# Optimization experiments

Hardware: AMD Instinct MI355X
Metric: run time of the kernel (lower is better)

## Reference

```python
import jax, jax.numpy as jnp
import numpy as np

N_NODES = 30000
N_EDGES = 240000
N_GRAPHS = 300
IN_CH = 5


def _bn(x, p):
    # inference batchnorm; p = stack([gamma, beta, running_mean, running_var]), shape (4, C)
    g, b, m, v = p
    return g * (x - m) * jax.lax.rsqrt(v + 1e-5) + b


def _gatv2(x, src, dst, wl, bl, wr, br, att, bias, heads, outc, concat):
    # PyG GATv2Conv: e_ij = att . leaky_relu(lin_l(x_j) + lin_r(x_i)), softmax over edges into i,
    # out_i = sum_j alpha_ij * lin_l(x_j)
    n = x.shape[0]
    xl = (x @ wl + bl).reshape(n, heads, outc)  # source-side transform
    xr = (x @ wr + br).reshape(n, heads, outc)  # target-side transform
    e = jax.nn.leaky_relu(xl[src] + xr[dst], 0.2)          # [E, H, C]
    logit = jnp.einsum('ehc,hc->eh', e, att)               # [E, H]
    lmax = jax.ops.segment_max(logit, dst, num_segments=n)
    lmax = jnp.where(jnp.isfinite(lmax), lmax, 0.0)        # empty segments -> 0
    ex = jnp.exp(logit - lmax[dst])
    den = jax.ops.segment_sum(ex, dst, num_segments=n)
    alpha = ex / (den[dst] + 1e-16)                        # PyG softmax eps
    out = jax.ops.segment_sum(xl[src] * alpha[..., None], dst, num_segments=n)
    out = out.reshape(n, heads * outc) if concat else out.mean(axis=1)
    return out + bias


def _forward(x, edge_index, batch, w_in, b_in, bn_in,
             g1_wl, g1_bl, g1_wr, g1_br, g1_att, g1_bias, bn1,
             g2_wl, g2_bl, g2_wr, g2_br, g2_att, g2_bias, bn2,
             g3_wl, g3_bl, g3_wr, g3_br, g3_att, g3_bias, bn3,
             c_w1, c_b1, c_bn, c_w2, c_b2, c_w3, c_b3):
    n = x.shape[0]
    loops = jnp.arange(n)
    src = jnp.concatenate([edge_index[0], loops])  # add_self_loops=True
    dst = jnp.concatenate([edge_index[1], loops])
    h = jax.nn.relu(_bn(x @ w_in + b_in, bn_in))
    h = jax.nn.elu(_bn(_gatv2(h, src, dst, g1_wl, g1_bl, g1_wr, g1_br, g1_att, g1_bias, 4, 64, True), bn1))
    h = jax.nn.elu(_bn(_gatv2(h, src, dst, g2_wl, g2_bl, g2_wr, g2_br, g2_att, g2_bias, 4, 64, True), bn2))
    h = jax.nn.elu(_bn(_gatv2(h, src, dst, g3_wl, g3_bl, g3_wr, g3_br, g3_att, g3_bias, 1, 128, False), bn3))
    cnt = jax.ops.segment_sum(jnp.ones((n,), h.dtype), batch, num_segments=N_GRAPHS)
    mean = jax.ops.segment_sum(h, batch, num_segments=N_GRAPHS) / jnp.maximum(cnt, 1.0)[:, None]
    mx = jax.ops.segment_max(h, batch, num_segments=N_GRAPHS)
    mx = jnp.where(jnp.isfinite(mx), mx, 0.0)
    g = jnp.concatenate([mean, mx], axis=1)                # (B, 256)
    z = jax.nn.relu(_bn(g @ c_w1 + c_b1, c_bn))
    z = jax.nn.relu(z @ c_w2 + c_b2)
    return jax.nn.log_softmax(z @ c_w3 + c_b3, axis=-1)    # (B, 2)


def setup_inputs() -> dict:
    base = jax.random.key(0)
    k = lambda i: jax.random.fold_in(base, i)
    def lin(i, fi, fo):
        return jax.random.normal(k(i), (fi, fo), jnp.float32) / np.sqrt(np.float32(fi))
    def vec(i, c):
        return jax.random.normal(k(i), (c,), jnp.float32) * 0.05
    def bn(i, c):
        g = jax.random.uniform(k(i), (c,), jnp.float32) + 0.5
        b = jax.random.normal(jax.random.fold_in(k(i), 1), (c,), jnp.float32) * 0.1
        return jnp.stack([g, b, jnp.zeros((c,), jnp.float32), jnp.ones((c,), jnp.float32)])
    def att(i, h, c):
        return jax.random.normal(k(i), (h, c), jnp.float32) / np.sqrt(np.float32(c))
    return dict(
        x=jax.random.normal(k(0), (N_NODES, IN_CH), jnp.float32),
        edge_index=jax.random.randint(k(1), (2, N_EDGES), 0, N_NODES),
        batch=jnp.sort(jax.random.randint(k(2), (N_NODES,), 0, N_GRAPHS)),
        w_in=lin(3, IN_CH, 64), b_in=vec(4, 64), bn_in=bn(5, 64),
        g1_wl=lin(6, 64, 256), g1_bl=vec(7, 256), g1_wr=lin(8, 64, 256), g1_br=vec(9, 256),
        g1_att=att(10, 4, 64), g1_bias=vec(11, 256), bn1=bn(12, 256),
        g2_wl=lin(13, 256, 256), g2_bl=vec(14, 256), g2_wr=lin(15, 256, 256), g2_br=vec(16, 256),
        g2_att=att(17, 4, 64), g2_bias=vec(18, 256), bn2=bn(19, 256),
        g3_wl=lin(20, 256, 128), g3_bl=vec(21, 128), g3_wr=lin(22, 256, 128), g3_br=vec(23, 128),
        g3_att=att(24, 1, 128), g3_bias=vec(25, 128), bn3=bn(26, 128),
        c_w1=lin(27, 256, 128), c_b1=vec(28, 128), c_bn=bn(29, 128),
        c_w2=lin(30, 128, 64), c_b2=vec(31, 64),
        c_w3=lin(32, 64, 2), c_b3=vec(33, 2),
    )


def reference(x, edge_index, batch, w_in, b_in, bn_in,
              g1_wl, g1_bl, g1_wr, g1_br, g1_att, g1_bias, bn1,
              g2_wl, g2_bl, g2_wr, g2_br, g2_att, g2_bias, bn2,
              g3_wl, g3_bl, g3_wr, g3_br, g3_att, g3_bias, bn3,
              c_w1, c_b1, c_bn, c_w2, c_b2, c_w3, c_b3):
    return _forward(x, edge_index, batch, w_in, b_in, bn_in,
                    g1_wl, g1_bl, g1_wr, g1_br, g1_att, g1_bias, bn1,
                    g2_wl, g2_bl, g2_wr, g2_br, g2_att, g2_bias, bn2,
                    g3_wl, g3_bl, g3_wr, g3_br, g3_att, g3_bias, bn3,
                    c_w1, c_b1, c_bn, c_w2, c_b2, c_w3, c_b3)
```

## Files before the change

### kernel.cpp

```cpp
#include <hip/hip_runtime.h>
#include <math.h>

#define N_NODES  30000
#define N_EDGES  240000
#define E_TOT    270000
#define N_GRAPHS 300
#define NCH      118

typedef _Float16 half8 __attribute__((ext_vector_type(8)));
typedef _Float16 half4 __attribute__((ext_vector_type(4)));
typedef float float4v __attribute__((ext_vector_type(4)));

static inline int cdiv(int a, int b) { return (a + b - 1) / b; }

static __device__ __forceinline__ void gload_lds16(const void* g, void* l) {
    __builtin_amdgcn_global_load_lds(
        (const __attribute__((address_space(1))) void*)g,
        (__attribute__((address_space(3))) void*)l, 16, 0, 0);
}

template<int CTRL>
static __device__ __forceinline__ float dpp_add(float v) {
    int t = __builtin_amdgcn_update_dpp(0, __float_as_int(v), CTRL, 0xF, 0xF, false);
    return v + __int_as_float(t);
}
static __device__ __forceinline__ float red16(float v) {
    v = dpp_add<0x128>(v);
    v = dpp_add<0x124>(v);
    v = dpp_add<0x122>(v);
    v = dpp_add<0x121>(v);
    return v;
}

__device__ inline void wp_dev(const float* __restrict__ W, _Float16* __restrict__ Wt,
                              int K, int CO, int gtid, int T) {
    int tot = K * CO;
    for (int i = gtid; i < tot; i += T) {
        int k = i / CO, c = i - k * CO;
        Wt[(size_t)c * K + k] = (_Float16)W[i];
    }
}

__global__ void hist_wprep_input(const int* __restrict__ ei, int* __restrict__ deg,
                                 const float* __restrict__ x, const float* __restrict__ w_in,
                                 const float* __restrict__ b_in, const float* __restrict__ bn_in,
                                 _Float16* __restrict__ a16,
                                 const float* __restrict__ w1l, const float* __restrict__ w1r,
                                 const float* __restrict__ w2l, const float* __restrict__ w2r,
                                 const float* __restrict__ w3l, const float* __restrict__ w3r,
                                 _Float16* __restrict__ t1l, _Float16* __restrict__ t1r,
                                 _Float16* __restrict__ t2l, _Float16* __restrict__ t2r,
                                 _Float16* __restrict__ t3l, _Float16* __restrict__ t3r) {
    int gtid = blockIdx.x * blockDim.x + threadIdx.x;
    int T = gridDim.x * blockDim.x;
    for (int e = gtid; e < E_TOT; e += T) {
        int d = (e < N_EDGES) ? ei[N_EDGES + e] : e - N_EDGES;
        atomicAdd(&deg[d], 1);
    }
    wp_dev(w1l, t1l, 64, 256, gtid, T);
    wp_dev(w1r, t1r, 64, 256, gtid, T);
    wp_dev(w2l, t2l, 256, 256, gtid, T);
    wp_dev(w2r, t2r, 256, 256, gtid, T);
    wp_dev(w3l, t3l, 256, 128, gtid, T);
    wp_dev(w3r, t3r, 256, 128, gtid, T);

    int lane = threadIdx.x & 63;
    int wv = blockIdx.x * (blockDim.x >> 6) + (threadIdx.x >> 6);
    int NW = gridDim.x * (blockDim.x >> 6);
    float g = bn_in[lane], be = bn_in[64 + lane];
    float m = bn_in[128 + lane], va = bn_in[192 + lane];
    float rs = rsqrtf(va + 1e-5f);
    float wcol[5];
#pragma unroll
    for (int ci = 0; ci < 5; ++ci) wcol[ci] = w_in[ci * 64 + lane];
    float bb = b_in[lane];
    for (int n = wv; n < N_NODES; n += NW) {
        float xv = (lane < 5) ? x[n * 5 + lane] : 0.f;
        float acc = bb;
#pragma unroll
        for (int ci = 0; ci < 5; ++ci)
            acc = fmaf(__shfl(xv, ci, 64), wcol[ci], acc);
        acc = g * (acc - m) * rs + be;
        a16[(size_t)n * 64 + lane] = (_Float16)fmaxf(acc, 0.f);
    }
}

__global__ __launch_bounds__(256)
void scan_all(const int* __restrict__ deg, const int* __restrict__ batch,
              int* __restrict__ row_start, int* __restrict__ gstart) {
    __shared__ int red[256];
    __shared__ int s[256];
    const int b = blockIdx.x, t = threadIdx.x;
    int pre = 0;
    for (int i = t; i < b * 256; i += 256) pre += deg[i];
    red[t] = pre;
    __syncthreads();
    for (int off = 128; off; off >>= 1) {
        if (t < off) red[t] += red[t + off];
        __syncthreads();
    }
    int base = red[0];
    int gid = b * 256 + t;
    int v = (gid < N_NODES) ? deg[gid] : 0;
    s[t] = v;
    __syncthreads();
    for (int off = 1; off < 256; off <<= 1) {
        int u = (t >= off) ? s[t - off] : 0;
        __syncthreads();
        s[t] += u;
        __syncthreads();
    }
    if (gid < N_NODES) row_start[gid] = base + s[t] - v;
    if (b == 0 && t == 0) row_start[N_NODES] = E_TOT;
    if (b == 0) {
        for (int g = t; g <= N_GRAPHS; g += 256) {
            int lo = 0, hi = N_NODES;
            while (lo < hi) {
                int mid = (lo + hi) >> 1;
                if (batch[mid] < g) lo = mid + 1;
                else                hi = mid;
            }
            gstart[g] = lo;
        }
    }
}

template<int K, int COUT, int SCAT>
__global__ __launch_bounds__(256, 4)
void gemm_mfma(const _Float16* __restrict__ A,
               const _Float16* __restrict__ Wtl, const float* __restrict__ bl,
               const _Float16* __restrict__ Wtr, const float* __restrict__ br,
               _Float16* __restrict__ outl, _Float16* __restrict__ outr,
               const int* __restrict__ ei, const int* __restrict__ row_start,
               int* __restrict__ cnt, int* __restrict__ esrc, int N) {
    constexpr int BM = 128, BN = 128, BK = 64;
    constexpr int CSL = COUT / BN > 0 ? COUT / BN : 1;
    constexpr int NS  = 2 * CSL;
    const int NT  = (N + BM - 1) / BM;
    const int nwg = NT * NS;
    const int id  = blockIdx.x;
    if (SCAT && id >= nwg) {
        int gtid = (id - nwg) * blockDim.x + threadIdx.x;
        int T = (gridDim.x - nwg) * blockDim.x;
        for (int e = gtid; e < E_TOT; e += T) {
            int s, d;
            if (e < N_EDGES) { s = ei[e]; d = ei[N_EDGES + e]; }
            else             { s = e - N_EDGES; d = s; }
            int slot = row_start[d] + atomicAdd(&cnt[d], 1);
            esrc[slot] = s;
        }
        return;
    }
    const int q = nwg >> 3, r = nwg & 7, xcd = id & 7, kk_ = id >> 3;
    const int rm = (xcd < r ? xcd * (q + 1) : r * (q + 1) + (xcd - r) * q) + kk_;
    const int tile = rm / NS, slice = rm % NS;

    __shared__ __attribute__((aligned(16))) _Float16 As[BM * BK];
    __shared__ __attribute__((aligned(16))) _Float16 Bs[BN * BK];
    const int tid  = threadIdx.x;
    const int wave = tid >> 6;
    const int lane = tid & 63;
    const int l15  = lane & 15;
    const int lq   = lane >> 4;
    const int n0   = tile * BM;
    const int sel  = slice / CSL;
    const int col0 = (slice % CSL) * BN;
    const _Float16* Wt = sel ? Wtr : Wtl;
    const float* bias  = sel ? br : bl;
    _Float16* out      = sel ? outr : outl;

    const int r0 = tid >> 3;
    const int us = (tid & 7) ^ (r0 & 7);

    float4v acc[2][8];
#pragma unroll
    for (int mi = 0; mi < 2; ++mi)
#pragma unroll
        for (int nt = 0; nt < 8; ++nt)
#pragma unroll
            for (int r2 = 0; r2 < 4; ++r2) acc[mi][nt][r2] = 0.f;

    for (int kt = 0; kt < K; kt += BK) {
#pragma unroll
        for (int p = 0; p < 4; ++p) {
            int row = p * 32 + r0;
            int gn  = n0 + row;
            if (gn >= N) gn = 0;
            gload_lds16(A + (size_t)gn * K + kt + us * 8, As + (p * 256 + tid) * 8);
        }
#pragma unroll
        for (int p = 0; p < 4; ++p) {
            int row = p * 32 + r0;
            gload_lds16(Wt + (size_t)(col0 + row) * K + kt + us * 8, Bs + (p * 256 + tid) * 8);
        }
        __syncthreads();
#pragma unroll
        for (int kk = 0; kk < BK; kk += 32) {
            const int sw = (lq + (kk >> 3)) ^ (l15 & 7);
            half8 af0 = *(const half8*)(As + (wave * 32 + l15) * BK + sw * 8);
            half8 af1 = *(const half8*)(As + (wave * 32 + 16 + l15) * BK + sw * 8);
#pragma unroll
            for (int nt = 0; nt < 8; ++nt) {
                half8 bf = *(const half8*)(Bs + (nt * 16 + l15) * BK + sw * 8);
                acc[0][nt] = __builtin_amdgcn_mfma_f32_16x16x32_f16(bf, af0, acc[0][nt], 0, 0, 0);
                acc[1][nt] = __builtin_amdgcn_mfma_f32_16x16x32_f16(bf, af1, acc[1][nt], 0, 0, 0);
            }
        }
        __syncthreads();
    }
#pragma unroll
    for (int mi = 0; mi < 2; ++mi) {
        int row = n0 + wave * 32 + mi * 16 + l15;
        if (row < N) {
#pragma unroll
            for (int nt = 0; nt < 8; ++nt) {
                int col = col0 + nt * 16 + lq * 4;
                float4v bv = *(const float4v*)(bias + col);
                half4 hv;
#pragma unroll
                for (int r2 = 0; r2 < 4; ++r2)
                    hv[r2] = (_Float16)(acc[mi][nt][r2] + bv[r2]);
                *(half4*)(out + (size_t)row * COUT + col) = hv;
            }
        }
    }
}

template<typename TOUT>
__global__ __launch_bounds__(256)
void gat_gather4(const _Float16* __restrict__ xl, const _Float16* __restrict__ xr,
                 const int* __restrict__ row_start, const int* __restrict__ esrc,
                 const float* __restrict__ att, const float* __restrict__ gbias,
                 const float* __restrict__ bnp, TOUT* __restrict__ out) {
    constexpr int HC = 256, PER = 4;
    int node = (blockIdx.x * blockDim.x + threadIdx.x) >> 6;
    int lane = threadIdx.x & 63;
    if (node >= N_NODES) return;
    const int base = lane * PER;

    float rr[PER], av[PER], acc[PER];
    {
        half4 rv = *(const half4*)(xr + (size_t)node * HC + base);
#pragma unroll
        for (int k = 0; k < PER; ++k) rr[k] = (float)rv[k];
        *(float4v*)av = *(const float4v*)(att + base);
    }
#pragma unroll
    for (int k = 0; k < PER; ++k) acc[k] = 0.f;

    float l = 0.f;
    const int j0 = row_start[node], j1 = row_start[node + 1];
    for (int jc = j0; jc < j1; jc += 64) {
        int nedge = min(64, j1 - jc);
        int ev = (jc + lane < j1) ? esrc[jc + lane] : 0;
        for (int jj = 0; jj < nedge; jj += 4) {
            int s[4];
            bool val[4];
#pragma unroll
            for (int u = 0; u < 4; ++u) {
                int idx = jj + u;
                val[u] = idx < nedge;
                s[u] = __shfl(ev, val[u] ? idx : jj, 64);
            }
            float xs[4][PER];
#pragma unroll
            for (int u = 0; u < 4; ++u) {
                half4 xv = *(const half4*)(xl + (size_t)s[u] * HC + base);
#pragma unroll
                for (int k = 0; k < PER; ++k) xs[u][k] = (float)xv[k];
            }
            float pz[4];
#pragma unroll
            for (int u = 0; u < 4; ++u) {
                float pp = 0.f;
#pragma unroll
                for (int k = 0; k < PER; ++k) {
                    float v = xs[u][k] + rr[k];
                    v = (v > 0.f) ? v : 0.2f * v;
                    pp = fmaf(v, av[k], pp);
                }
                pz[u] = red16(pp);
            }
            float w[4];
#pragma unroll
            for (int u = 0; u < 4; ++u) w[u] = val[u] ? __expf(pz[u]) : 0.f;
            l += (w[0] + w[1]) + (w[2] + w[3]);
#pragma unroll
            for (int k = 0; k < PER; ++k)
                acc[k] += fmaf(w[0], xs[0][k],
                          fmaf(w[1], xs[1][k],
                          fmaf(w[2], xs[2][k], w[3] * xs[3][k])));
        }
    }
    float inv = 1.f / (l + 1e-16f);
    float o[PER];
#pragma unroll
    for (int k = 0; k < PER; ++k) {
        float v = fmaf(acc[k], inv, gbias[base + k]);
        float g  = bnp[base + k], be = bnp[HC + base + k];
        float mm = bnp[2 * HC + base + k], va = bnp[3 * HC + base + k];
        v = g * (v - mm) * rsqrtf(va + 1e-5f) + be;
        o[k] = (v > 0.f) ? v : (__expf(v) - 1.f);
    }
    half4 ov;
#pragma unroll
    for (int k = 0; k < PER; ++k) ov[k] = (_Float16)o[k];
    *(half4*)((_Float16*)out + (size_t)node * HC + base) = ov;
}

__global__ __launch_bounds__(256)
void gat_gather1(const _Float16* __restrict__ xl, const _Float16* __restrict__ xr,
                 const int* __restrict__ row_start, const int* __restrict__ esrc,
                 const float* __restrict__ att, const float* __restrict__ gbias,
                 const float* __restrict__ bnp, float* __restrict__ out) {
    constexpr int HC = 128, PER = 4;
    int node = (blockIdx.x * blockDim.x + threadIdx.x) >> 6;
    int lane = threadIdx.x & 63;
    if (node >= N_NODES) return;
    const int half = lane >> 5;
    const int base = (lane & 31) * PER;

    float rr[PER], av[PER], acc[PER];
    {
        half4 rv = *(const half4*)(xr + (size_t)node * HC + base);
#pragma unroll
        for (int k = 0; k < PER; ++k) rr[k] = (float)rv[k];
        *(float4v*)av = *(const float4v*)(att + base);
    }
#pragma unroll
    for (int k = 0; k < PER; ++k) acc[k] = 0.f;

    float l = 0.f;
    const int j0 = row_start[node], j1 = row_start[node + 1];
    for (int jc = j0; jc < j1; jc += 64) {
        int nedge = min(64, j1 - jc);
        int ev = (jc + lane < j1) ? esrc[jc + lane] : 0;
        for (int jj = 0; jj < nedge; jj += 8) {
            int s[4];
            bool val[4];
#pragma unroll
            for (int u = 0; u < 4; ++u) {
                int idx = jj + 2 * u + half;
                val[u] = idx < nedge;
                s[u] = __shfl(ev, val[u] ? idx : jj, 64);
            }
            float xs[4][PER];
#pragma unroll
            for (int u = 0; u < 4; ++u) {
                half4 xv = *(const half4*)(xl + (size_t)s[u] * HC + base);
#pragma unroll
                for (int k = 0; k < PER; ++k) xs[u][k] = (float)xv[k];
            }
            float pz[4];
#pragma unroll
            for (int u = 0; u < 4; ++u) {
                float pp = 0.f;
#pragma unroll
                for (int k = 0; k < PER; ++k) {
                    float v = xs[u][k] + rr[k];
                    v = (v > 0.f) ? v : 0.2f * v;
                    pp = fmaf(v, av[k], pp);
                }
                pp += __shfl_xor(pp, 16, 64);
                pz[u] = red16(pp);
            }
            float w[4];
#pragma unroll
            for (int u = 0; u < 4; ++u) w[u] = val[u] ? __expf(pz[u]) : 0.f;
            l += (w[0] + w[1]) + (w[2] + w[3]);
#pragma unroll
            for (int k = 0; k < PER; ++k)
                acc[k] += fmaf(w[0], xs[0][k],
                          fmaf(w[1], xs[1][k],
                          fmaf(w[2], xs[2][k], w[3] * xs[3][k])));
        }
    }
    l += __shfl_xor(l, 32, 64);
#pragma unroll
    for (int k = 0; k < PER; ++k) acc[k] += __shfl_xor(acc[k], 32, 64);

    if (half == 0) {
        float inv = 1.f / (l + 1e-16f);
        float o[PER];
#pragma unroll
        for (int k = 0; k < PER; ++k) {
            float v = fmaf(acc[k], inv, gbias[base + k]);
            float g  = bnp[base + k], be = bnp[HC + base + k];
            float mm = bnp[2 * HC + base + k], va = bnp[3 * HC + base + k];
            v = g * (v - mm) * rsqrtf(va + 1e-5f) + be;
            o[k] = (v > 0.f) ? v : (__expf(v) - 1.f);
        }
        *(float4v*)(out + (size_t)node * HC + base) = *(float4v*)o;
    }
}

__global__ __launch_bounds__(512)
void pool_cls(const float* __restrict__ h, const int* __restrict__ gstart,
              const float* __restrict__ w1, const float* __restrict__ b1,
              const float* __restrict__ bnp,
              const float* __restrict__ w2, const float* __restrict__ b2,
              const float* __restrict__ w3, const float* __restrict__ b3,
              float* __restrict__ out) {
    __shared__ float part[512];
    __shared__ float sg[256];
    __shared__ float sz1[128];
    __shared__ float sz2[64];
    __shared__ float sz3[2];
    int g = blockIdx.x, t = threadIdx.x;
    int c = t & 127, q = t >> 7;
    int a = gstart[g], b = gstart[g + 1];
    float sum = 0.f, mx = -INFINITY;
    for (int i = a + q; i < b; i += 4) {
        float v = h[(size_t)i * 128 + c];
        sum += v;
        mx = fmaxf(mx, v);
    }
    part[t] = sum;
    __syncthreads();
    if (q == 0)
        sg[c] = (part[c] + part[c + 128] + part[c + 256] + part[c + 384])
                / fmaxf((float)(b - a), 1.f);
    __syncthreads();
    part[t] = mx;
    __syncthreads();
    if (q == 0) {
        float m2 = fmaxf(fmaxf(part[c], part[c + 128]),
                         fmaxf(part[c + 256], part[c + 384]));
        sg[128 + c] = (b > a) ? m2 : 0.f;
    }
    __syncthreads();
    float acc = 0.f;
    for (int i = q * 64; i < q * 64 + 64; ++i) acc += sg[i] * w1[i * 128 + c];
    part[t] = acc;
    __syncthreads();
    if (q == 0) {
        float z = part[c] + part[c + 128] + part[c + 256] + part[c + 384] + b1[c];
        float ga = bnp[c], be = bnp[128 + c], m = bnp[256 + c], va = bnp[384 + c];
        z = ga * (z - m) * rsqrtf(va + 1e-5f) + be;
        sz1[c] = fmaxf(z, 0.f);
    }
    __syncthreads();
    if (t < 128) {
        int o = t & 63, q2 = t >> 6;
        float a2 = 0.f;
        for (int i = q2 * 64; i < q2 * 64 + 64; ++i) a2 += sz1[i] * w2[i * 64 + o];
        part[t] = a2;
    }
    __syncthreads();
    if (t < 64) sz2[t] = fmaxf(part[t] + part[t + 64] + b2[t], 0.f);
    __syncthreads();
    if (t < 2) {
        float a3 = b3[t];
        for (int i = 0; i < 64; ++i) a3 += sz2[i] * w3[i * 2 + t];
        sz3[t] = a3;
    }
    __syncthreads();
    if (t < 2) {
        float mm = fmaxf(sz3[0], sz3[1]);
        float lse = mm + logf(expf(sz3[0] - mm) + expf(sz3[1] - mm));
        out[g * 2 + t] = sz3[t] - lse;
    }
}

extern "C" void kernel_launch(void* const* d_in, const int* in_sizes, int n_in,
                              void* d_out, int out_size, void* d_ws, size_t ws_size,
                              hipStream_t stream) {
    const float* x       = (const float*)d_in[0];
    const int*   ei      = (const int*)d_in[1];
    const int*   batch   = (const int*)d_in[2];
    const float* w_in    = (const float*)d_in[3];
    const float* b_in    = (const float*)d_in[4];
    const float* bn_in   = (const float*)d_in[5];
    const float* g1_wl   = (const float*)d_in[6];
    const float* g1_bl   = (const float*)d_in[7];
    const float* g1_wr   = (const float*)d_in[8];
    const float* g1_br   = (const float*)d_in[9];
    const float* g1_att  = (const float*)d_in[10];
    const float* g1_bias = (const float*)d_in[11];
    const float* bn1     = (const float*)d_in[12];
    const float* g2_wl   = (const float*)d_in[13];
    const float* g2_bl   = (const float*)d_in[14];
    const float* g2_wr   = (const float*)d_in[15];
    const float* g2_br   = (const float*)d_in[16];
    const float* g2_att  = (const float*)d_in[17];
    const float* g2_bias = (const float*)d_in[18];
    const float* bn2     = (const float*)d_in[19];
    const float* g3_wl   = (const float*)d_in[20];
    const float* g3_bl   = (const float*)d_in[21];
    const float* g3_wr   = (const float*)d_in[22];
    const float* g3_br   = (const float*)d_in[23];
    const float* g3_att  = (const float*)d_in[24];
    const float* g3_bias = (const float*)d_in[25];
    const float* bn3     = (const float*)d_in[26];
    const float* c_w1    = (const float*)d_in[27];
    const float* c_b1    = (const float*)d_in[28];
    const float* c_bn    = (const float*)d_in[29];
    const float* c_w2    = (const float*)d_in[30];
    const float* c_b2    = (const float*)d_in[31];
    const float* c_w3    = (const float*)d_in[32];
    const float* c_b3    = (const float*)d_in[33];
    float* out = (float*)d_out;

    const size_t NHC = (size_t)N_NODES * 256;
    _Float16* a16  = (_Float16*)d_ws;
    _Float16* xl16 = a16 + NHC;
    _Float16* xr16 = xl16 + NHC;
    _Float16* wt = xr16 + NHC;
    _Float16* wt1l = wt;            _Float16* wt1r = wt + 16384;
    _Float16* wt2l = wt + 32768;    _Float16* wt2r = wt + 98304;
    _Float16* wt3l = wt + 163840;   _Float16* wt3r = wt + 196608;
    float* fbase = (float*)(wt + 262144);
    float* bufD = fbase;
    int* iw = (int*)(bufD + (size_t)N_NODES * 128);
    int* deg       = iw;            int* cnt    = iw + 30000;
    int* row_start = iw + 90128;
    int* esrc      = iw + 120129;
    int* gstart    = iw + 390429;

    const int BT = 256;
    const int NT128 = cdiv(N_NODES, 128);

    hipMemsetAsync(deg, 0, 60000 * sizeof(int), stream);

    hist_wprep_input<<<1024, BT, 0, stream>>>(ei, deg, x, w_in, b_in, bn_in, a16,
                                              g1_wl, g1_wr, g2_wl, g2_wr, g3_wl, g3_wr,
                                              wt1l, wt1r, wt2l, wt2r, wt3l, wt3r);
    scan_all<<<NCH, 256, 0, stream>>>(deg, batch, row_start, gstart);

    gemm_mfma<64, 256, 1><<<NT128 * 4 + NT128, 256, 0, stream>>>(
        a16, wt1l, g1_bl, wt1r, g1_br, xl16, xr16, ei, row_start, cnt, esrc, N_NODES);
    gat_gather4<_Float16><<<cdiv(N_NODES * 64, BT), BT, 0, stream>>>(
        xl16, xr16, row_start, esrc, g1_att, g1_bias, bn1, a16);

    gemm_mfma<256, 256, 0><<<NT128 * 4, 256, 0, stream>>>(
        a16, wt2l, g2_bl, wt2r, g2_br, xl16, xr16, nullptr, nullptr, nullptr, nullptr, N_NODES);
    gat_gather4<_Float16><<<cdiv(N_NODES * 64, BT), BT, 0, stream>>>(
        xl16, xr16, row_start, esrc, g2_att, g2_bias, bn2, a16);

    gemm_mfma<256, 128, 0><<<NT128 * 2, 256, 0, stream>>>(
        a16, wt3l, g3_bl, wt3r, g3_br, xl16, xr16, nullptr, nullptr, nullptr, nullptr, N_NODES);
    gat_gather1<<<cdiv(N_NODES * 64, BT), BT, 0, stream>>>(
        xl16, xr16, row_start, esrc, g3_att, g3_bias, bn3, bufD);

    pool_cls<<<N_GRAPHS, 512, 0, stream>>>(bufD, gstart, c_w1, c_b1, c_bn,
                                           c_w2, c_b2, c_w3, c_b3, out);
}
```

Measured before the change: 309.5 us.

## Move layer-2/3 weight prep into scatter blocks, vectorize scan, coalesce transpose writes

The fp16 transposes of the layer-2 and layer-3 weights move out of the histogram/input kernel and into the spare edge-scatter blocks of the first GEMM launch, taking them off the critical path of the initial kernel. The weight transpose now iterates over output order, so the fp16 writes are coalesced and the fp32 reads become strided. The prefix sum in scan_all reads degrees as int4 vectors, and the leaky-ReLU select becomes a single fmax. The trade-off is more work inside the scatter blocks of the first GEMM launch, which could lengthen that kernel.

```diff
diff --git a/kernel.cpp b/kernel.cpp
--- a/kernel.cpp
+++ b/kernel.cpp
@@ -36,8 +36,8 @@
                               int K, int CO, int gtid, int T) {
     int tot = K * CO;
     for (int i = gtid; i < tot; i += T) {
-        int k = i / CO, c = i - k * CO;
-        Wt[(size_t)c * K + k] = (_Float16)W[i];
+        int c = i / K, k = i - c * K;
+        Wt[i] = (_Float16)W[(size_t)k * CO + c];
     }
 }
 
@@ -46,11 +46,7 @@
                                  const float* __restrict__ b_in, const float* __restrict__ bn_in,
                                  _Float16* __restrict__ a16,
                                  const float* __restrict__ w1l, const float* __restrict__ w1r,
-                                 const float* __restrict__ w2l, const float* __restrict__ w2r,
-                                 const float* __restrict__ w3l, const float* __restrict__ w3r,
-                                 _Float16* __restrict__ t1l, _Float16* __restrict__ t1r,
-                                 _Float16* __restrict__ t2l, _Float16* __restrict__ t2r,
-                                 _Float16* __restrict__ t3l, _Float16* __restrict__ t3r) {
+                                 _Float16* __restrict__ t1l, _Float16* __restrict__ t1r) {
     int gtid = blockIdx.x * blockDim.x + threadIdx.x;
     int T = gridDim.x * blockDim.x;
     for (int e = gtid; e < E_TOT; e += T) {
@@ -59,10 +55,6 @@
     }
     wp_dev(w1l, t1l, 64, 256, gtid, T);
     wp_dev(w1r, t1r, 64, 256, gtid, T);
-    wp_dev(w2l, t2l, 256, 256, gtid, T);
-    wp_dev(w2r, t2r, 256, 256, gtid, T);
-    wp_dev(w3l, t3l, 256, 128, gtid, T);
-    wp_dev(w3r, t3r, 256, 128, gtid, T);
 
     int lane = threadIdx.x & 63;
     int wv = blockIdx.x * (blockDim.x >> 6) + (threadIdx.x >> 6);
@@ -91,8 +83,12 @@
     __shared__ int red[256];
     __shared__ int s[256];
     const int b = blockIdx.x, t = threadIdx.x;
+    const int4* deg4 = (const int4*)deg;
     int pre = 0;
-    for (int i = t; i < b * 256; i += 256) pre += deg[i];
+    for (int i = t; i < b * 64; i += 256) {
+        int4 v4 = deg4[i];
+        pre += (v4.x + v4.y) + (v4.z + v4.w);
+    }
     red[t] = pre;
     __syncthreads();
     for (int off = 128; off; off >>= 1) {
@@ -132,7 +128,11 @@
                const _Float16* __restrict__ Wtr, const float* __restrict__ br,
                _Float16* __restrict__ outl, _Float16* __restrict__ outr,
                const int* __restrict__ ei, const int* __restrict__ row_start,
-               int* __restrict__ cnt, int* __restrict__ esrc, int N) {
+               int* __restrict__ cnt, int* __restrict__ esrc, int N,
+               const float* __restrict__ w2l, const float* __restrict__ w2r,
+               const float* __restrict__ w3l, const float* __restrict__ w3r,
+               _Float16* __restrict__ t2l, _Float16* __restrict__ t2r,
+               _Float16* __restrict__ t3l, _Float16* __restrict__ t3r) {
     constexpr int BM = 128, BN = 128, BK = 64;
     constexpr int CSL = COUT / BN > 0 ? COUT / BN : 1;
     constexpr int NS  = 2 * CSL;
@@ -149,6 +149,10 @@
             int slot = row_start[d] + atomicAdd(&cnt[d], 1);
             esrc[slot] = s;
         }
+        wp_dev(w2l, t2l, 256, 256, gtid, T);
+        wp_dev(w2r, t2r, 256, 256, gtid, T);
+        wp_dev(w3l, t3l, 256, 128, gtid, T);
+        wp_dev(w3r, t3r, 256, 128, gtid, T);
         return;
     }
     const int q = nwg >> 3, r = nwg & 7, xcd = id & 7, kk_ = id >> 3;
@@ -276,7 +280,7 @@
 #pragma unroll
                 for (int k = 0; k < PER; ++k) {
                     float v = xs[u][k] + rr[k];
-                    v = (v > 0.f) ? v : 0.2f * v;
+                    v = fmaxf(v, 0.2f * v);
                     pp = fmaf(v, av[k], pp);
                 }
                 pz[u] = red16(pp);
@@ -358,7 +362,7 @@
 #pragma unroll
                 for (int k = 0; k < PER; ++k) {
                     float v = xs[u][k] + rr[k];
-                    v = (v > 0.f) ? v : 0.2f * v;
+                    v = fmaxf(v, 0.2f * v);
                     pp = fmaf(v, av[k], pp);
                 }
                 pp += __shfl_xor(pp, 16, 64);
@@ -523,22 +527,24 @@
     hipMemsetAsync(deg, 0, 60000 * sizeof(int), stream);
 
     hist_wprep_input<<<1024, BT, 0, stream>>>(ei, deg, x, w_in, b_in, bn_in, a16,
-                                              g1_wl, g1_wr, g2_wl, g2_wr, g3_wl, g3_wr,
-                                              wt1l, wt1r, wt2l, wt2r, wt3l, wt3r);
+                                              g1_wl, g1_wr, wt1l, wt1r);
     scan_all<<<NCH, 256, 0, stream>>>(deg, batch, row_start, gstart);
 
     gemm_mfma<64, 256, 1><<<NT128 * 4 + NT128, 256, 0, stream>>>(
-        a16, wt1l, g1_bl, wt1r, g1_br, xl16, xr16, ei, row_start, cnt, esrc, N_NODES);
+        a16, wt1l, g1_bl, wt1r, g1_br, xl16, xr16, ei, row_start, cnt, esrc, N_NODES,
+        g2_wl, g2_wr, g3_wl, g3_wr, wt2l, wt2r, wt3l, wt3r);
     gat_gather4<_Float16><<<cdiv(N_NODES * 64, BT), BT, 0, stream>>>(
         xl16, xr16, row_start, esrc, g1_att, g1_bias, bn1, a16);
 
     gemm_mfma<256, 256, 0><<<NT128 * 4, 256, 0, stream>>>(
-        a16, wt2l, g2_bl, wt2r, g2_br, xl16, xr16, nullptr, nullptr, nullptr, nullptr, N_NODES);
+        a16, wt2l, g2_bl, wt2r, g2_br, xl16, xr16, nullptr, nullptr, nullptr, nullptr, N_NODES,
+        nullptr, nullptr, nullptr, nullptr, nullptr, nullptr, nullptr, nullptr);
     gat_gather4<_Float16><<<cdiv(N_NODES * 64, BT), BT, 0, stream>>>(
         xl16, xr16, row_start, esrc, g2_att, g2_bias, bn2, a16);
 
     gemm_mfma<256, 128, 0><<<NT128 * 2, 256, 0, stream>>>(
-        a16, wt3l, g3_bl, wt3r, g3_br, xl16, xr16, nullptr, nullptr, nullptr, nullptr, N_NODES);
+        a16, wt3l, g3_bl, wt3r, g3_br, xl16, xr16, nullptr, nullptr, nullptr, nullptr, N_NODES,
+        nullptr, nullptr, nullptr, nullptr, nullptr, nullptr, nullptr, nullptr);
     gat_gather1<<<cdiv(N_NODES * 64, BT), BT, 0, stream>>>(
         xl16, xr16, row_start, esrc, g3_att, g3_bias, bn3, bufD);
 
```

Result: no change. 306.7 us (-0.9%).
